# Kernel tuning notes

Hardware: AMD Instinct MI355X
Metric: run time of the kernel (lower is better)

The kernel has to match this reference:

```python
import jax, jax.numpy as jnp
import numpy as np

L, H, D, DK, FF = 3, 8, 128, 16, 512  # layers, heads, embed, key/val dim, ffn hidden
B, N, F_IN, OUT = 32, 512, 16, 3
SCALE = 1.0 / np.sqrt(DK)


def setup_inputs() -> dict:
    key = jax.random.key(0)
    ks = jax.random.split(key, 16)
    x = jax.random.normal(ks[0], (B, N, F_IN), dtype=jnp.float32)
    m = jax.random.randint(ks[1], (B, N, N), 0, 2).astype(jnp.int32)
    # guarantee each query attends to at least itself (avoid all -inf rows)
    m = jnp.maximum(m, jnp.eye(N, dtype=jnp.int32)[None])
    def u(k, shape, fan):
        s = 1.0 / np.sqrt(fan)
        return jax.random.uniform(k, shape, jnp.float32, -s, s)
    return {
        "x": x, "mask": m,
        "We": u(ks[2], (F_IN, D), D),
        "Wq": u(ks[3], (L, H, D, DK), DK),
        "Wk": u(ks[4], (L, H, D, DK), DK),
        "Wv": u(ks[5], (L, H, D, DK), DK),
        "Wout": u(ks[6], (L, H, DK, D), D),
        "Wff1": u(ks[7], (L, D, FF), D),
        "bff1": u(ks[8], (L, FF), D),
        "Wff2": u(ks[9], (L, FF, D), FF),
        "bff2": u(ks[10], (L, D), FF),
        "Wp": u(ks[11], (D, D), D),
        "Wr": u(ks[12], (2 * D, OUT), 2 * D),
        "br": u(ks[13], (OUT,), 2 * D),
    }


def reference(x, mask, We, Wq, Wk, Wv, Wout, Wff1, bff1, Wff2, bff2, Wp, Wr, br):
    mb = mask.astype(bool)[None]  # [1,B,N,N] broadcast over heads
    h = jax.nn.relu(x @ We)  # initial embedding [B,N,D]
    for l in range(L):
        # multi-head attention with additive skip
        Q = jnp.einsum('bnd,hdk->hbnk', h, Wq[l])
        K = jnp.einsum('bnd,hdk->hbnk', h, Wk[l])
        V = jnp.einsum('bnd,hdk->hbnk', h, Wv[l])
        compat = SCALE * jnp.einsum('hbqk,hbnk->hbqn', Q, K)  # [H,B,N,N]
        compat = jnp.where(mb, compat, -jnp.inf)
        attn = jax.nn.softmax(compat, axis=-1)
        # note: torch's attn.clone()[...] = 0 is a no-op, so no re-zeroing
        heads = jnp.einsum('hbqn,hbnk->hbqk', attn, V)
        h = h + jnp.einsum('hbqk,hkd->bqd', heads, Wout[l])
        # feed-forward with additive skip
        h = h + jax.nn.relu(h @ Wff1[l] + bff1[l]) @ Wff2[l] + bff2[l] * 0 + (jax.nn.relu(h @ Wff1[l] + bff1[l]) @ Wff2[l] + bff2[l] - (jax.nn.relu(h @ Wff1[l] + bff1[l]) @ Wff2[l]))  # placeholder removed below
    return h


# clean faithful version (used)
def reference(x, mask, We, Wq, Wk, Wv, Wout, Wff1, bff1, Wff2, bff2, Wp, Wr, br):
    mb = mask.astype(bool)[None]  # [1,B,N,N]
    h = jax.nn.relu(x @ We)  # [B,N,D]
    for l in range(L):
        Q = jnp.einsum('bnd,hdk->hbnk', h, Wq[l])
        K = jnp.einsum('bnd,hdk->hbnk', h, Wk[l])
        V = jnp.einsum('bnd,hdk->hbnk', h, Wv[l])
        compat = SCALE * jnp.einsum('hbqk,hbnk->hbqn', Q, K)
        compat = jnp.where(mb, compat, -jnp.inf)
        attn = jax.nn.softmax(compat, axis=-1)
        heads = jnp.einsum('hbqn,hbnk->hbqk', attn, V)
        h = h + jnp.einsum('hbqk,hkd->bqd', heads, Wout[l])
        h = h + (jax.nn.relu(h @ Wff1[l] + bff1[l]) @ Wff2[l] + bff2[l])
    # readout (actor head: output_dim=3)
    h_pooled = (h.mean(axis=1)) @ Wp  # [B,D]
    f_pooled = jnp.broadcast_to(h_pooled[:, None, :], h.shape)  # [B,N,D]
    features = jax.nn.relu(jnp.concatenate([f_pooled, h], axis=-1))  # [B,N,2D]
    return features @ Wr + br  # [B,N,3]
```

## Files before the change

### kernel.cpp

```cpp
#include <hip/hip_runtime.h>
#include <cstdint>
#include <cstddef>

#define L_LAYERS 3
#define H_HEADS 8
#define D_EMB 128
#define DKV 16
#define FF_DIM 512
#define B_BATCH 32
#define N_SEQ 512
#define F_INP 16
#define OUT_DIM 3
#define M_ROWS (B_BATCH * N_SEQ)

typedef unsigned short ushort_t;
typedef unsigned int uint_t;
typedef __attribute__((ext_vector_type(8))) short short8;
typedef __attribute__((ext_vector_type(4))) float f32x4;
typedef __attribute__((ext_vector_type(16))) float f32x16;

__device__ inline ushort_t f2bf(float x) {
    union { float f; uint_t u; } v; v.f = x;
    uint_t r = v.u + 0x7fffu + ((v.u >> 16) & 1u);
    return (ushort_t)(r >> 16);
}

__device__ inline uint_t pack2bf(float a, float b) {
    union { float f; uint_t u; } ua, ub;
    ua.f = a; ub.f = b;
    uint_t ra = ua.u + 0x7fffu + ((ua.u >> 16) & 1u);
    uint_t rb = ub.u + 0x7fffu + ((ub.u >> 16) & 1u);
    return (ra >> 16) | (rb & 0xffff0000u);
}

__device__ inline void gload16(const void* g, void* l) {
    __builtin_amdgcn_global_load_lds(
        (const __attribute__((address_space(1))) unsigned int*)g,
        (__attribute__((address_space(3))) unsigned int*)l, 16, 0, 0);
}

#define PM_BLK 32768
#define RQ_BLK 576
#define TW_BLK 192
#define T1_BLK 768
#define T2_BLK 768
#define PB_BLK 16
#define EM_BLK 8192
__global__ __launch_bounds__(256) void preproc_kernel(
        const int* __restrict__ mask, unsigned long long* __restrict__ pm,
        const float* __restrict__ Wq, const float* __restrict__ Wk,
        const float* __restrict__ Wv, ushort_t* __restrict__ wqkvT,
        const float* __restrict__ Wout, ushort_t* __restrict__ woutT,
        const float* __restrict__ Wff1, ushort_t* __restrict__ wff1T,
        const float* __restrict__ Wff2, ushort_t* __restrict__ wff2T,
        float* __restrict__ pbsum,
        const float* __restrict__ x, const float* __restrict__ We,
        float* __restrict__ hf, ushort_t* __restrict__ hb) {
    int bx = blockIdx.x;
    const int tid = threadIdx.x;
    if (bx < PM_BLK) {
        int gid = bx * 256 + tid;
        int v = mask[gid];
        unsigned long long bal = __ballot(v != 0);
        if ((tid & 63) == 0) pm[gid >> 6] = bal;
        return;
    }
    bx -= PM_BLK;
    if (bx < RQ_BLK) {
        int idx = bx * 256 + tid;
        int d = idx & 127;
        int n = (idx >> 7) % 384;
        int l = idx / (384 * 128);
        int proj = n >> 7, hh = (n & 127) >> 4, kk = n & 15;
        const float* src = proj == 0 ? Wq : proj == 1 ? Wk : Wv;
        wqkvT[idx] = f2bf(src[((size_t)(l * 8 + hh) * 128 + d) * 16 + kk]);
        return;
    }
    bx -= RQ_BLK;
    if (bx < TW_BLK + T1_BLK + T2_BLK) {
        const float* src; ushort_t* dst; int R, C;
        if (bx < TW_BLK) { src = Wout; dst = woutT; R = 128; C = 128; }
        else if (bx < TW_BLK + T1_BLK) { src = Wff1; dst = wff1T; R = 128; C = 512; bx -= TW_BLK; }
        else { src = Wff2; dst = wff2T; R = 512; C = 128; bx -= TW_BLK + T1_BLK; }
        int idx = bx * 256 + tid;
        int b = idx / (R * C);
        int rem = idx - b * (R * C);
        int r = rem / C, c = rem - r * C;
        dst[(size_t)b * R * C + (size_t)c * R + r] = f2bf(src[idx]);
        return;
    }
    bx -= TW_BLK + T1_BLK + T2_BLK;
    if (bx < PB_BLK) {
        pbsum[bx * 256 + tid] = 0.f;
        return;
    }
    bx -= PB_BLK;
    {
        const int d = tid & 127;
        const int m = bx * 2 + (tid >> 7);
        const float* xr = x + (size_t)m * 16;
        float acc = 0.f;
#pragma unroll
        for (int k = 0; k < 16; k++) acc += xr[k] * We[k * 128 + d];
        acc = fmaxf(acc, 0.f);
        hf[(size_t)m * 128 + d] = acc;
        hb[(size_t)m * 128 + d] = f2bf(acc);
    }
}

__global__ __launch_bounds__(512, 2) void qkv_attn_kernel(
        const ushort_t* __restrict__ hb,
        const ushort_t* __restrict__ WqkvT,
        const uint_t* __restrict__ pm,
        ushort_t* __restrict__ Aout) {
    __shared__ __align__(16) ushort_t sm[29824];
    ushort_t* Qs  = sm;
    ushort_t* KF  = sm + 4096;
    ushort_t* Vt  = sm + 12288;
    ushort_t* Ws  = sm + 20608;
    ushort_t* Ps  = sm + 20608;

    const int tid = threadIdx.x;
    const int w = tid >> 6, L = tid & 63;
    const int lr = L & 15, lq = L >> 4;
    const int lane31 = L & 31, lhalf = L >> 5;
    const int bx = blockIdx.x;
    const int b = bx >> 4, h = (bx >> 1) & 7, half = bx & 1;

    for (int i = tid; i < 768; i += 512) {
        const int row = i >> 4, cg = i & 15;
        const int proj = row >> 4, kk = row & 15;
        gload16(WqkvT + (size_t)(proj * 128 + h * 16 + kk) * 128 + cg * 8, &Ws[i * 8]);
    }
    __syncthreads();

    const ushort_t* Ab = hb + (size_t)b * 512 * 128;
    for (int mc = 0; mc < 4; mc++) {
        f32x4 acc[3];
#pragma unroll
        for (int j = 0; j < 3; j++) acc[j] = (f32x4){0.f, 0.f, 0.f, 0.f};
#pragma unroll
        for (int k0 = 0; k0 < 128; k0 += 32) {
            short8 af = *(const short8*)(Ab + (size_t)(mc * 128 + w * 16 + lr) * 128 + k0 + lq * 8);
#pragma unroll
            for (int j = 0; j < 3; j++) {
                short8 bf = *(const short8*)&Ws[(j * 16 + lr) * 128 + k0 + lq * 8];
                acc[j] = __builtin_amdgcn_mfma_f32_16x16x32_bf16(af, bf, acc[j], 0, 0, 0);
            }
        }
        const int rbase = mc * 128 + w * 16 + lq * 4;
#pragma unroll
        for (int r = 0; r < 4; r++) {
            const int key = rbase + r;
            KF[(key >> 5) * 512 + ((lr >> 3) * 32 + (key & 31)) * 8 + (lr & 7)] = f2bf(acc[1][r]);
            Vt[lr * 520 + key] = f2bf(acc[2][r]);
        }
        if ((mc >> 1) == half) {
            const int qb = (mc & 1) * 128 + w * 16 + lq * 4;
#pragma unroll
            for (int r = 0; r < 4; r++)
                Qs[(qb + r) * 16 + lr] = f2bf(acc[0][r] * 0.25f);
        }
    }
    __syncthreads();

    const int q0g = half * 256 + w * 32;
    const short8 qf = *(const short8*)&Qs[(w * 32 + lane31) * 16 + lhalf * 8];
    const uint_t* pmr = pm + (size_t)(b * 512 + q0g + lane31) * 16;
    const uint4 mwa = *(const uint4*)(pmr);
    const uint4 mwb = *(const uint4*)(pmr + 4);
    const uint4 mwc = *(const uint4*)(pmr + 8);
    const uint4 mwd = *(const uint4*)(pmr + 12);
    const uint_t mw[16] = {mwa.x, mwa.y, mwa.z, mwa.w, mwb.x, mwb.y, mwb.z, mwb.w,
                           mwc.x, mwc.y, mwc.z, mwc.w, mwd.x, mwd.y, mwd.z, mwd.w};
    const f32x16 zero16 = (f32x16)(0.f);

    float mx = -1e30f;
#pragma unroll
    for (int t = 0; t < 16; t++) {
        short8 kf = *(const short8*)&KF[t * 512 + L * 8];
        f32x16 s = __builtin_amdgcn_mfma_f32_32x32x16_bf16(kf, qf, zero16, 0, 0, 0);
#pragma unroll
        for (int r = 0; r < 16; r++) mx = fmaxf(mx, s[r]);
    }
    mx = fmaxf(mx, __shfl_xor(mx, 32));

    float lsum = 0.f;
    f32x4 oacc0 = (f32x4){0.f, 0.f, 0.f, 0.f};
    f32x4 oacc1 = (f32x4){0.f, 0.f, 0.f, 0.f};
#pragma unroll
    for (int t = 0; t < 16; t++) {
        short8 kf = *(const short8*)&KF[t * 512 + L * 8];
        f32x16 s = __builtin_amdgcn_mfma_f32_32x32x16_bf16(kf, qf, zero16, 0, 0, 0);
        const uint_t word = mw[t];
#pragma unroll
        for (int r = 0; r < 16; r++) {
            const int keyl = (r & 3) + 8 * (r >> 2) + 4 * lhalf;
            const float e = __expf(s[r] - mx);
            const float pv = (word & (1u << keyl)) ? e : 0.f;
            s[r] = pv;
            lsum += pv;
        }
#pragma unroll
        for (int g = 0; g < 4; g++) {
            const uint_t lo = pack2bf(s[g * 4 + 0], s[g * 4 + 1]);
            const uint_t hi = pack2bf(s[g * 4 + 2], s[g * 4 + 3]);
            *(uint2*)&Ps[w * 1152 + lane31 * 36 + g * 8 + 4 * lhalf] = make_uint2(lo, hi);
        }
        short8 vb = *(const short8*)&Vt[lr * 520 + t * 32 + lq * 8];
        short8 pa0 = *(const short8*)&Ps[w * 1152 + lr * 36 + lq * 8];
        short8 pa1 = *(const short8*)&Ps[w * 1152 + (16 + lr) * 36 + lq * 8];
        oacc0 = __builtin_amdgcn_mfma_f32_16x16x32_bf16(pa0, vb, oacc0, 0, 0, 0);
        oacc1 = __builtin_amdgcn_mfma_f32_16x16x32_bf16(pa1, vb, oacc1, 0, 0, 0);
    }
    lsum += __shfl_xor(lsum, 32);

#pragma unroll
    for (int qa = 0; qa < 2; qa++) {
        const f32x4 oa = qa ? oacc1 : oacc0;
#pragma unroll
        for (int rr = 0; rr < 4; rr++) {
            const int qloc = qa * 16 + lq * 4 + rr;
            const float ls = __shfl(lsum, qloc, 64);
            Aout[(size_t)(b * 512 + q0g + qloc) * 128 + h * 16 + lr] = f2bf(oa[rr] / ls);
        }
    }
}

__global__ __launch_bounds__(256, 2) void tail_kernel(
        const ushort_t* __restrict__ A,
        const ushort_t* __restrict__ WoT,
        const ushort_t* __restrict__ W1T,
        const ushort_t* __restrict__ W2T,
        const float* __restrict__ b1,
        const float* __restrict__ b2,
        float* __restrict__ hf, ushort_t* __restrict__ hb,
        float* __restrict__ pbsum, int accum) {
    __shared__ __align__(16) ushort_t sm[38400];
    ushort_t* As  = sm;
    ushort_t* Bs  = sm + 1024;
    ushort_t* C1b = sm + 17408;
    ushort_t* T   = sm + 21760;

    const int tid = threadIdx.x;
    const int w = tid >> 6, l = tid & 63;
    const int lr = l & 15, lq = l >> 4;
    const int srow = (l >> 2);
    const int scol = (l & 3) * 8;
    const int m0 = blockIdx.x * 32;

    f32x4 c1a[2][2];
#pragma unroll
    for (int i = 0; i < 2; i++)
#pragma unroll
        for (int j = 0; j < 2; j++) c1a[i][j] = (f32x4){0.f, 0.f, 0.f, 0.f};
    for (int k0 = 0; k0 < 128; k0 += 32) {
        if (w < 2)
            gload16(A + (size_t)(m0 + w * 16 + srow) * 128 + k0 + scol,
                    &As[(w * 16 + srow) * 32 + scol]);
#pragma unroll
        for (int it = 0; it < 2; it++)
            gload16(WoT + (size_t)(it * 64 + w * 16 + srow) * 128 + k0 + scol,
                    &Bs[(it * 64 + w * 16 + srow) * 32 + scol]);
        __syncthreads();
        short8 af[2], bfr[2];
#pragma unroll
        for (int i = 0; i < 2; i++) af[i] = *(const short8*)&As[(i * 16 + lr) * 32 + lq * 8];
#pragma unroll
        for (int j = 0; j < 2; j++) bfr[j] = *(const short8*)&Bs[(w * 32 + j * 16 + lr) * 32 + lq * 8];
#pragma unroll
        for (int i = 0; i < 2; i++)
#pragma unroll
            for (int j = 0; j < 2; j++)
                c1a[i][j] = __builtin_amdgcn_mfma_f32_16x16x32_bf16(af[i], bfr[j], c1a[i][j], 0, 0, 0);
        __syncthreads();
    }
    float c1[2][2][4];
#pragma unroll
    for (int i = 0; i < 2; i++)
#pragma unroll
        for (int r = 0; r < 4; r++) {
            const int row = i * 16 + lq * 4 + r;
#pragma unroll
            for (int j = 0; j < 2; j++) {
                const int n = w * 32 + j * 16 + lr;
                const float v = c1a[i][j][r] + hf[(size_t)(m0 + row) * 128 + n];
                c1[i][j][r] = v;
                C1b[row * 136 + n] = f2bf(v);
            }
        }
    __syncthreads();

    f32x4 ta[2][8];
#pragma unroll
    for (int i = 0; i < 2; i++)
#pragma unroll
        for (int j = 0; j < 8; j++) ta[i][j] = (f32x4){0.f, 0.f, 0.f, 0.f};
    for (int k0 = 0; k0 < 128; k0 += 32) {
#pragma unroll
        for (int it = 0; it < 8; it++)
            gload16(W1T + (size_t)(it * 64 + w * 16 + srow) * 128 + k0 + scol,
                    &Bs[(it * 64 + w * 16 + srow) * 32 + scol]);
        __syncthreads();
        short8 af[2], bfr[8];
#pragma unroll
        for (int i = 0; i < 2; i++) af[i] = *(const short8*)&C1b[(i * 16 + lr) * 136 + k0 + lq * 8];
#pragma unroll
        for (int j = 0; j < 8; j++) bfr[j] = *(const short8*)&Bs[(w * 128 + j * 16 + lr) * 32 + lq * 8];
#pragma unroll
        for (int i = 0; i < 2; i++)
#pragma unroll
            for (int j = 0; j < 8; j++)
                ta[i][j] = __builtin_amdgcn_mfma_f32_16x16x32_bf16(af[i], bfr[j], ta[i][j], 0, 0, 0);
        __syncthreads();
    }
#pragma unroll
    for (int j = 0; j < 8; j++) {
        const int n = w * 128 + j * 16 + lr;
        const float bv = b1[n];
#pragma unroll
        for (int i = 0; i < 2; i++)
#pragma unroll
            for (int r = 0; r < 4; r++) {
                const int row = i * 16 + lq * 4 + r;
                T[row * 520 + n] = f2bf(fmaxf(ta[i][j][r] + bv, 0.f));
            }
    }
    __syncthreads();

    f32x4 oa[2][2];
#pragma unroll
    for (int i = 0; i < 2; i++)
#pragma unroll
        for (int j = 0; j < 2; j++) oa[i][j] = (f32x4){0.f, 0.f, 0.f, 0.f};
    for (int k0 = 0; k0 < 512; k0 += 32) {
#pragma unroll
        for (int it = 0; it < 2; it++)
            gload16(W2T + (size_t)(it * 64 + w * 16 + srow) * 512 + k0 + scol,
                    &Bs[(it * 64 + w * 16 + srow) * 32 + scol]);
        __syncthreads();
        short8 af[2], bfr[2];
#pragma unroll
        for (int i = 0; i < 2; i++) af[i] = *(const short8*)&T[(i * 16 + lr) * 520 + k0 + lq * 8];
#pragma unroll
        for (int j = 0; j < 2; j++) bfr[j] = *(const short8*)&Bs[(w * 32 + j * 16 + lr) * 32 + lq * 8];
#pragma unroll
        for (int i = 0; i < 2; i++)
#pragma unroll
            for (int j = 0; j < 2; j++)
                oa[i][j] = __builtin_amdgcn_mfma_f32_16x16x32_bf16(af[i], bfr[j], oa[i][j], 0, 0, 0);
        __syncthreads();
    }
#pragma unroll
    for (int j = 0; j < 2; j++) {
        const int n = w * 32 + j * 16 + lr;
        const float bv = b2[n];
        float psum = 0.f;
#pragma unroll
        for (int i = 0; i < 2; i++)
#pragma unroll
            for (int r = 0; r < 4; r++) {
                const int row = i * 16 + lq * 4 + r;
                const float v = oa[i][j][r] + bv + c1[i][j][r];
                psum += v;
                hf[(size_t)(m0 + row) * 128 + n] = v;
                hb[(size_t)(m0 + row) * 128 + n] = f2bf(v);
            }
        if (accum) {
            psum += __shfl_xor(psum, 16);
            psum += __shfl_xor(psum, 32);
            if (lq == 0) atomicAdd(&pbsum[(m0 >> 9) * 128 + n], psum);
        }
    }
}

__global__ __launch_bounds__(256) void readout_kernel(const float* __restrict__ h,
                                                      const float* __restrict__ pbsum,
                                                      const float* __restrict__ Wp,
                                                      const float* __restrict__ Wr,
                                                      const float* __restrict__ br,
                                                      float* __restrict__ out) {
    const int u = blockIdx.x;
    const int b = u >> 4;
    const int m0 = u * 32;
    const int t = threadIdx.x;
    __shared__ float pooled[128];
    __shared__ float rp[128];
    __shared__ float pb3[3];
    if (t < 128) pooled[t] = pbsum[b * 128 + t] * (1.0f / 512.0f);
    __syncthreads();
    if (t < 128) {
        float a = 0.f;
        for (int dd = 0; dd < 128; dd++) a += pooled[dd] * Wp[dd * 128 + t];
        rp[t] = fmaxf(a, 0.f);
    }
    __syncthreads();
    if (t < OUT_DIM) {
        float a = br[t];
        for (int j = 0; j < 128; j++) a += rp[j] * Wr[j * 3 + t];
        pb3[t] = a;
    }
    __syncthreads();
    const int j = t & 7;
    const int row = m0 + (t >> 3);
    const float* hr = h + (size_t)row * 128 + j * 16;
    float a0 = 0.f, a1 = 0.f, a2o = 0.f;
#pragma unroll
    for (int dd = 0; dd < 16; dd++) {
        const float v = fmaxf(hr[dd], 0.f);
        const float* wr = Wr + (size_t)(128 + j * 16 + dd) * 3;
        a0 += v * wr[0]; a1 += v * wr[1]; a2o += v * wr[2];
    }
#pragma unroll
    for (int off = 4; off; off >>= 1) {
        a0 += __shfl_down(a0, off, 8);
        a1 += __shfl_down(a1, off, 8);
        a2o += __shfl_down(a2o, off, 8);
    }
    if (j == 0) {
        out[(size_t)row * 3 + 0] = a0 + pb3[0];
        out[(size_t)row * 3 + 1] = a1 + pb3[1];
        out[(size_t)row * 3 + 2] = a2o + pb3[2];
    }
}

extern "C" void kernel_launch(void* const* d_in, const int* in_sizes, int n_in,
                              void* d_out, int out_size, void* d_ws, size_t ws_size,
                              hipStream_t stream) {
    const float* x    = (const float*)d_in[0];
    const int*   mask = (const int*)d_in[1];
    const float* We   = (const float*)d_in[2];
    const float* Wq   = (const float*)d_in[3];
    const float* Wk   = (const float*)d_in[4];
    const float* Wv   = (const float*)d_in[5];
    const float* Wout = (const float*)d_in[6];
    const float* Wff1 = (const float*)d_in[7];
    const float* bff1 = (const float*)d_in[8];
    const float* Wff2 = (const float*)d_in[9];
    const float* bff2 = (const float*)d_in[10];
    const float* Wp   = (const float*)d_in[11];
    const float* Wr   = (const float*)d_in[12];
    const float* br   = (const float*)d_in[13];
    float* out = (float*)d_out;

    char* ws = (char*)d_ws;
    unsigned long long* pm64 = (unsigned long long*)(ws + 0);
    const uint_t* pm32       = (const uint_t*)(ws + 0);
    ushort_t* wqkvT = (ushort_t*)(ws + 1048576);
    ushort_t* woutT = (ushort_t*)(ws + 1343488);
    ushort_t* wff1T = (ushort_t*)(ws + 1441792);
    ushort_t* wff2T = (ushort_t*)(ws + 1835008);
    float*    pbsum = (float*)(ws + 2228224);
    float*    hbuf  = (float*)(ws + 4194304);
    ushort_t* hb16  = (ushort_t*)(ws + 12582912);
    ushort_t* a16   = (ushort_t*)(ws + 41943040);

    preproc_kernel<<<PM_BLK + RQ_BLK + TW_BLK + T1_BLK + T2_BLK + PB_BLK + EM_BLK, 256, 0, stream>>>(
        mask, pm64, Wq, Wk, Wv, wqkvT, Wout, woutT, Wff1, wff1T, Wff2, wff2T,
        pbsum, x, We, hbuf, hb16);

    for (int l = 0; l < L_LAYERS; l++) {
        qkv_attn_kernel<<<512, 512, 0, stream>>>(
            hb16, wqkvT + (size_t)l * 384 * 128, pm32, a16);
        tail_kernel<<<M_ROWS / 32, 256, 0, stream>>>(
            a16, woutT + (size_t)l * 128 * 128, wff1T + (size_t)l * 512 * 128,
            wff2T + (size_t)l * 128 * 512, bff1 + l * 512, bff2 + l * 128,
            hbuf, hb16, pbsum, (l == L_LAYERS - 1) ? 1 : 0);
    }

    readout_kernel<<<512, 256, 0, stream>>>(hbuf, pbsum, Wp, Wr, br, out);
}
```

Before: 297.3 us.

## Load MFMA weight and activation fragments directly from global memory instead of LDS staging

Weight tiles in the QKV/attention kernel and the tail (Wout, FF1, FF2) kernel are no longer staged through shared memory. Each lane now reads its short8 MFMA operand straight from global memory (L1/L2-cached), and the per-k-step __syncthreads barriers are dropped. Shared memory in the tail kernel shrinks to the C1 and T buffers, which may allow more resident blocks. In exchange, global loads become uncoalesced and per-lane, and weight fragments are re-read by every wave, so latency could be exposed.

```diff
diff --git a/kernel.cpp b/kernel.cpp
--- a/kernel.cpp
+++ b/kernel.cpp
@@ -117,7 +117,6 @@
     ushort_t* Qs  = sm;
     ushort_t* KF  = sm + 4096;
     ushort_t* Vt  = sm + 12288;
-    ushort_t* Ws  = sm + 20608;
     ushort_t* Ps  = sm + 20608;
 
     const int tid = threadIdx.x;
@@ -127,13 +126,6 @@
     const int bx = blockIdx.x;
     const int b = bx >> 4, h = (bx >> 1) & 7, half = bx & 1;
 
-    for (int i = tid; i < 768; i += 512) {
-        const int row = i >> 4, cg = i & 15;
-        const int proj = row >> 4, kk = row & 15;
-        gload16(WqkvT + (size_t)(proj * 128 + h * 16 + kk) * 128 + cg * 8, &Ws[i * 8]);
-    }
-    __syncthreads();
-
     const ushort_t* Ab = hb + (size_t)b * 512 * 128;
     for (int mc = 0; mc < 4; mc++) {
         f32x4 acc[3];
@@ -144,7 +136,7 @@
             short8 af = *(const short8*)(Ab + (size_t)(mc * 128 + w * 16 + lr) * 128 + k0 + lq * 8);
 #pragma unroll
             for (int j = 0; j < 3; j++) {
-                short8 bf = *(const short8*)&Ws[(j * 16 + lr) * 128 + k0 + lq * 8];
+                short8 bf = *(const short8*)(WqkvT + (size_t)(j * 128 + h * 16 + lr) * 128 + k0 + lq * 8);
                 acc[j] = __builtin_amdgcn_mfma_f32_16x16x32_bf16(af, bf, acc[j], 0, 0, 0);
             }
         }
@@ -236,17 +228,12 @@
         const float* __restrict__ b2,
         float* __restrict__ hf, ushort_t* __restrict__ hb,
         float* __restrict__ pbsum, int accum) {
-    __shared__ __align__(16) ushort_t sm[38400];
-    ushort_t* As  = sm;
-    ushort_t* Bs  = sm + 1024;
-    ushort_t* C1b = sm + 17408;
-    ushort_t* T   = sm + 21760;
+    __shared__ __align__(16) ushort_t C1b[32 * 136];
+    __shared__ __align__(16) ushort_t T[32 * 520];
 
     const int tid = threadIdx.x;
     const int w = tid >> 6, l = tid & 63;
     const int lr = l & 15, lq = l >> 4;
-    const int srow = (l >> 2);
-    const int scol = (l & 3) * 8;
     const int m0 = blockIdx.x * 32;
 
     f32x4 c1a[2][2];
@@ -254,26 +241,20 @@
     for (int i = 0; i < 2; i++)
 #pragma unroll
         for (int j = 0; j < 2; j++) c1a[i][j] = (f32x4){0.f, 0.f, 0.f, 0.f};
+#pragma unroll
     for (int k0 = 0; k0 < 128; k0 += 32) {
-        if (w < 2)
-            gload16(A + (size_t)(m0 + w * 16 + srow) * 128 + k0 + scol,
-                    &As[(w * 16 + srow) * 32 + scol]);
-#pragma unroll
-        for (int it = 0; it < 2; it++)
-            gload16(WoT + (size_t)(it * 64 + w * 16 + srow) * 128 + k0 + scol,
-                    &Bs[(it * 64 + w * 16 + srow) * 32 + scol]);
-        __syncthreads();
         short8 af[2], bfr[2];
 #pragma unroll
-        for (int i = 0; i < 2; i++) af[i] = *(const short8*)&As[(i * 16 + lr) * 32 + lq * 8];
-#pragma unroll
-        for (int j = 0; j < 2; j++) bfr[j] = *(const short8*)&Bs[(w * 32 + j * 16 + lr) * 32 + lq * 8];
+        for (int i = 0; i < 2; i++)
+            af[i] = *(const short8*)(A + (size_t)(m0 + i * 16 + lr) * 128 + k0 + lq * 8);
+#pragma unroll
+        for (int j = 0; j < 2; j++)
+            bfr[j] = *(const short8*)(WoT + (size_t)(w * 32 + j * 16 + lr) * 128 + k0 + lq * 8);
 #pragma unroll
         for (int i = 0; i < 2; i++)
 #pragma unroll
             for (int j = 0; j < 2; j++)
                 c1a[i][j] = __builtin_amdgcn_mfma_f32_16x16x32_bf16(af[i], bfr[j], c1a[i][j], 0, 0, 0);
-        __syncthreads();
     }
     float c1[2][2][4];
 #pragma unroll
@@ -296,23 +277,20 @@
     for (int i = 0; i < 2; i++)
 #pragma unroll
         for (int j = 0; j < 8; j++) ta[i][j] = (f32x4){0.f, 0.f, 0.f, 0.f};
+#pragma unroll
     for (int k0 = 0; k0 < 128; k0 += 32) {
-#pragma unroll
-        for (int it = 0; it < 8; it++)
-            gload16(W1T + (size_t)(it * 64 + w * 16 + srow) * 128 + k0 + scol,
-                    &Bs[(it * 64 + w * 16 + srow) * 32 + scol]);
-        __syncthreads();
         short8 af[2], bfr[8];
 #pragma unroll
-        for (int i = 0; i < 2; i++) af[i] = *(const short8*)&C1b[(i * 16 + lr) * 136 + k0 + lq * 8];
-#pragma unroll
-        for (int j = 0; j < 8; j++) bfr[j] = *(const short8*)&Bs[(w * 128 + j * 16 + lr) * 32 + lq * 8];
+        for (int i = 0; i < 2; i++)
+            af[i] = *(const short8*)&C1b[(i * 16 + lr) * 136 + k0 + lq * 8];
+#pragma unroll
+        for (int j = 0; j < 8; j++)
+            bfr[j] = *(const short8*)(W1T + (size_t)(w * 128 + j * 16 + lr) * 128 + k0 + lq * 8);
 #pragma unroll
         for (int i = 0; i < 2; i++)
 #pragma unroll
             for (int j = 0; j < 8; j++)
                 ta[i][j] = __builtin_amdgcn_mfma_f32_16x16x32_bf16(af[i], bfr[j], ta[i][j], 0, 0, 0);
-        __syncthreads();
     }
 #pragma unroll
     for (int j = 0; j < 8; j++) {
@@ -333,23 +311,20 @@
     for (int i = 0; i < 2; i++)
 #pragma unroll
         for (int j = 0; j < 2; j++) oa[i][j] = (f32x4){0.f, 0.f, 0.f, 0.f};
+#pragma unroll
     for (int k0 = 0; k0 < 512; k0 += 32) {
-#pragma unroll
-        for (int it = 0; it < 2; it++)
-            gload16(W2T + (size_t)(it * 64 + w * 16 + srow) * 512 + k0 + scol,
-                    &Bs[(it * 64 + w * 16 + srow) * 32 + scol]);
-        __syncthreads();
         short8 af[2], bfr[2];
 #pragma unroll
-        for (int i = 0; i < 2; i++) af[i] = *(const short8*)&T[(i * 16 + lr) * 520 + k0 + lq * 8];
-#pragma unroll
-        for (int j = 0; j < 2; j++) bfr[j] = *(const short8*)&Bs[(w * 32 + j * 16 + lr) * 32 + lq * 8];
+        for (int i = 0; i < 2; i++)
+            af[i] = *(const short8*)&T[(i * 16 + lr) * 520 + k0 + lq * 8];
+#pragma unroll
+        for (int j = 0; j < 2; j++)
+            bfr[j] = *(const short8*)(W2T + (size_t)(w * 32 + j * 16 + lr) * 512 + k0 + lq * 8);
 #pragma unroll
         for (int i = 0; i < 2; i++)
 #pragma unroll
             for (int j = 0; j < 2; j++)
                 oa[i][j] = __builtin_amdgcn_mfma_f32_16x16x32_bf16(af[i], bfr[j], oa[i][j], 0, 0, 0);
-        __syncthreads();
     }
 #pragma unroll
     for (int j = 0; j < 2; j++) {
```

Result: slower. 320.7 us (+7.9%).
